# Kernel tuning notes

Hardware: AMD Instinct MI355X
Metric: run time of the kernel (lower is better)

The kernel has to match this reference:

```python
import jax, jax.numpy as jnp
import numpy as np

INF = 1e5
EPS = 1e-8
SCALE = 0.1            # coordinate_scaling
VFN_F = 1.0            # vfn_attn_factor
DIST_F = 1.0           # dist_attn_factor
AFS = VFN_F + DIST_F + 2.0  # attn_factor_sum
B, N, CS, H, C, P, PV, K, G = 2, 512, 384, 12, 16, 8, 8, 16, 64


def quat_to_rot(q):
    q = q / jnp.linalg.norm(q, axis=-1, keepdims=True)
    w, x, y, z = q[..., 0], q[..., 1], q[..., 2], q[..., 3]
    R = jnp.stack([
        1 - 2 * (y * y + z * z), 2 * (x * y - w * z), 2 * (x * z + w * y),
        2 * (x * y + w * z), 1 - 2 * (x * x + z * z), 2 * (y * z - w * x),
        2 * (x * z - w * y), 2 * (y * z + w * x), 1 - 2 * (x * x + y * y)], axis=-1)
    return R.reshape(q.shape[:-1] + (3, 3))


def layer_norm(x, g, b):
    m = jnp.mean(x, -1, keepdims=True)
    v = jnp.mean((x - m) ** 2, -1, keepdims=True)
    return (x - m) * jax.lax.rsqrt(v + 1e-5) * g + b


def setup_inputs() -> dict:
    key = jax.random.key(0)
    ks = jax.random.split(key, 32)
    w = lambda k, shape, sc=0.02: jax.random.normal(k, shape, jnp.float32) * sc
    s = jax.random.normal(ks[0], (B, N, CS), jnp.float32)
    rot = quat_to_rot(jax.random.normal(ks[1], (B, N, 4), jnp.float32))
    trans = jax.random.normal(ks[2], (B, N, 3), jnp.float32) * 10.0
    mask = jnp.ones((B, N), jnp.float32)
    return dict(
        s=s, rot=rot, trans=trans, mask=mask,
        Wq=w(ks[3], (CS, H * C)), bq=jnp.zeros((H * C,), jnp.float32),
        Wkv=w(ks[4], (CS, 2 * H * C)), bkv=jnp.zeros((2 * H * C,), jnp.float32),
        head_weights=jnp.full((H,), 0.5413, jnp.float32),
        ln_g=jnp.ones((CS,), jnp.float32), ln_b=jnp.zeros((CS,), jnp.float32),
        Wpq=w(ks[5], (CS, P * 3)), bpq=jnp.zeros((P * 3,), jnp.float32),
        Wpv=w(ks[6], (CS, P * 3)), bpv=jnp.zeros((P * 3,), jnp.float32),
        Wvl=w(ks[7], (P, 2 * P), 0.1),
        gbf_means=jnp.linspace(0.0, 3.0, K).astype(jnp.float32),
        gbf_stds=jnp.linspace(0.5, 2.0, K).astype(jnp.float32),
        Wg=w(ks[8], (P * K, G)), bg=jnp.zeros((G,), jnp.float32),
        W1=w(ks[9], (G, G)), b1=jnp.zeros((G,), jnp.float32),
        W2=w(ks[10], (G, H)), b2=jnp.zeros((H,), jnp.float32),
        Wkvp=w(ks[11], (CS, H * PV * 3)), bkvp=jnp.zeros((H * PV * 3,), jnp.float32),
        Wout=w(ks[12], (H * (C + 4 * PV), CS)), bout=jnp.zeros((CS,), jnp.float32),
    )


def reference(s, rot, trans, mask, Wq, bq, Wkv, bkv, head_weights, ln_g, ln_b,
              Wpq, bpq, Wpv, bpv, Wvl, gbf_means, gbf_stds, Wg, bg,
              W1, b1, W2, b2, Wkvp, bkvp, Wout, bout):
    # pairwise squared distances on scaled coordinates -> per-head distance bias
    coord = trans * SCALE
    diff = coord[:, None, :, :] - coord[:, :, None, :]
    pair_dist = jnp.sum(diff * diff, -1)                      # [B,N,N]
    hw = jax.nn.softplus(head_weights) * ((1.0 / (AFS * 4.5)) ** 0.5) * -0.5
    dist_att = pair_dist[..., None] * hw                      # [B,N,N,H]

    # scalar q/k/v
    q = (s @ Wq + bq).reshape(B, N, H, C)
    kv = (s @ Wkv + bkv).reshape(B, N, H, 2 * C)
    k, v = kv[..., :C], kv[..., C:]

    # VFN point features from layer-normed s
    sn = layer_norm(s, ln_g, ln_b)
    q_pts = (sn @ Wpq + bpq).reshape(B, N, P, 3)
    v_pts = (sn @ Wpv + bpv).reshape(B, N, P, 3)

    # relative rigid T_i^{-1} o T_j applied to v_pts of residue j
    R_rel = jnp.einsum('biyx,bjyz->bijxz', rot, rot)          # R_i^T R_j [B,N,N,3,3]
    dt = trans[:, None, :, :] - trans[:, :, None, :]          # t_j - t_i
    t_rel = jnp.einsum('biyx,bijy->bijx', rot, dt)            # R_i^T (t_j - t_i)
    v_loc = jnp.einsum('bijxy,bjpy->bijpx', R_rel, v_pts) + t_rel[:, :, :, None, :]
    q_rep = jnp.broadcast_to(q_pts[:, :, None], (B, N, N, P, 3))
    vin = jnp.concatenate([v_loc, q_rep], axis=-2)            # [B,N,N,2P,3]
    vec = jnp.einsum('op,bijpc->bijoc', Wvl, vin) + v_loc     # equivariant VecLinear + residual
    vlen = jnp.sqrt(jnp.sum(vec * vec, -1) + EPS)             # [B,N,N,P]

    # Gaussian basis expansion then pair MLP -> per-head VFN attention bias
    gauss = jnp.exp(-0.5 * ((vlen[..., None] - gbf_means) / gbf_stds) ** 2)  # [B,N,N,P,K]
    g = gauss.reshape(B, N, N, P * K) @ Wg + bg               # [B,N,N,G]
    vfn = jax.nn.relu(g @ W1 + b1) @ W2 + b2                  # [B,N,N,H]

    # fused attention logits
    a = jnp.einsum('bihc,bjhc->bhij', q, k) * ((1.0 / (AFS * C)) ** 0.5)
    a = a + jnp.transpose(vfn, (0, 3, 1, 2)) * (VFN_F / (AFS ** 0.5))
    a = a + jnp.transpose(dist_att, (0, 3, 1, 2)) * DIST_F
    sq_mask = INF * (mask[:, :, None] * mask[:, None, :] - 1.0)
    a = jax.nn.softmax(a + sq_mask[:, None], axis=-1)         # [B,H,N,N]

    # scalar output
    o = jnp.einsum('bhij,bjhc->bihc', a, v).reshape(B, N, H * C)

    # point values in global (scaled) frame, aggregate, back to local frame
    kv_pts = (s @ Wkvp + bkvp).reshape(B, N, H * PV, 3)
    ts = trans * SCALE
    vg = (jnp.einsum('bixy,biky->bikx', rot, kv_pts) + ts[:, :, None, :]).reshape(B, N, H, PV, 3)
    o_pt = jnp.einsum('bhij,bjhpc->bihpc', a, vg)             # [B,N,H,PV,3]
    o_loc = jnp.einsum('biyx,bihpy->bihpx', rot, o_pt - ts[:, :, None, None, :])
    dists = jnp.sqrt(jnp.sum(o_loc * o_loc, -1) + EPS).reshape(B, N, H * PV)
    pts = o_loc.reshape(B, N, H * PV, 3)
    feats = jnp.concatenate([o, pts[..., 0], pts[..., 1], pts[..., 2], dists], axis=-1)
    s_out = feats @ Wout + bout                               # [B,N,CS]
    return s_out, g
```

## Files before the change

### kernel.cpp

```cpp
#include <hip/hip_runtime.h>
#include <math.h>

#define BB 2
#define NN 512
#define CSZ 384
#define HH 12
#define CC 16
#define PP 8
#define PVV 8
#define KG 16
#define GG 64
#define NCOL 912
#define NODES (BB*NN)

typedef __attribute__((ext_vector_type(8))) short bf16x8;
typedef __attribute__((ext_vector_type(4))) float floatx4;

__device__ __forceinline__ unsigned short f2bf(float x) {
  unsigned u = __float_as_uint(x);
  unsigned r = (u + 0x7FFF + ((u >> 16) & 1)) >> 16;
  return (unsigned short)r;
}

__global__ void k0_prep(const float* __restrict__ Wq, const float* __restrict__ Wkv,
                        const float* __restrict__ Wpq, const float* __restrict__ Wpv,
                        const float* __restrict__ Wkvp,
                        const float* __restrict__ bq, const float* __restrict__ bkv,
                        const float* __restrict__ bpq, const float* __restrict__ bpv,
                        const float* __restrict__ bkvp,
                        const float* __restrict__ ln_g, const float* __restrict__ ln_b,
                        const float* __restrict__ W1, const float* __restrict__ hwin,
                        const float* __restrict__ Wg, const float* __restrict__ W2,
                        float* __restrict__ Wbig, float* __restrict__ biasbig,
                        float* __restrict__ P2big, unsigned short* __restrict__ wbf,
                        float* __restrict__ hw)
{
  int idx = blockIdx.x*blockDim.x + threadIdx.x;
  int stride = gridDim.x*blockDim.x;
  for (int t = idx; t < CSZ*NCOL; t += stride) {
    int f = t / NCOL, c = t % NCOL;
    float w;
    if (c < 192)      w = Wq[f*192 + c];
    else if (c < 576) w = Wkv[f*384 + (c-192)];
    else if (c < 600) w = ln_g[f]*Wpq[f*24 + (c-576)];
    else if (c < 624) w = ln_g[f]*Wpv[f*24 + (c-600)];
    else              w = Wkvp[f*288 + (c-624)];
    Wbig[t] = w;
  }
  for (int t = idx; t < 8192; t += stride) {
    int ch = t >> 7, pk = t & 127;
    float wv = Wg[pk*64 + ch];
    unsigned short h = f2bf(wv);
    float hf = __uint_as_float(((unsigned)h) << 16);
    wbf[t] = h;
    wbf[8192 + t] = f2bf(wv - hf);
  }
  for (int t = idx; t < 4096; t += stride) {
    int ho = t >> 6, k = t & 63;
    wbf[16384 + t] = f2bf(W1[k*64 + ho]);
  }
  for (int t = idx; t < 1024; t += stride) {
    int hh = t >> 6, ho = t & 63;
    wbf[20480 + t] = (hh < 12) ? f2bf(W2[ho*12 + hh]) : (unsigned short)0;
  }
  for (int c = idx; c < NCOL; c += stride) {
    float bb, p2 = 0.f;
    if (c < 192)      bb = bq[c];
    else if (c < 576) bb = bkv[c-192];
    else if (c < 624) {
      const float* W = (c < 600) ? (Wpq + (c-576)) : (Wpv + (c-600));
      float p1 = 0.f;
      for (int f = 0; f < CSZ; ++f) { p1 += ln_b[f]*W[f*24]; p2 += ln_g[f]*W[f*24]; }
      bb = ((c < 600) ? bpq[c-576] : bpv[c-600]) + p1;
    }
    else bb = bkvp[c-624];
    biasbig[c] = bb; P2big[c] = p2;
  }
  for (int h = idx; h < HH; h += stride) {
    float x = hwin[h];
    float sp = (x > 20.f) ? x : log1pf(expf(x));
    hw[h] = sp * sqrtf(1.0f/18.0f) * -0.5f;
  }
}

__global__ void k0b_stats(const float* __restrict__ s, float* __restrict__ mout,
                          float* __restrict__ rstdout)
{
  int node = blockIdx.x;
  int l = threadIdx.x;
  const float* row = s + node*CSZ;
  float sum = 0.f, sum2 = 0.f;
  for (int f = l; f < CSZ; f += 64) { float v = row[f]; sum += v; sum2 += v*v; }
  #pragma unroll
  for (int off = 1; off < 64; off <<= 1) { sum += __shfl_xor(sum, off); sum2 += __shfl_xor(sum2, off); }
  if (l == 0) {
    float m = sum / CSZ;
    float var = sum2 / CSZ - m*m;
    mout[node] = m;
    rstdout[node] = rsqrtf(var + 1e-5f);
  }
}

__launch_bounds__(256)
__global__ void k1_gemm(const float* __restrict__ s, const float* __restrict__ Wbig,
                        const float* __restrict__ biasbig, const float* __restrict__ P2big,
                        const float* __restrict__ mrow, const float* __restrict__ rstd,
                        float* __restrict__ act)
{
  const int ROWS = 4;
  int row0 = blockIdx.x * ROWS;
  int t = threadIdx.x;
  float acc[4][ROWS];
  #pragma unroll
  for (int j = 0; j < 4; ++j)
    #pragma unroll
    for (int r = 0; r < ROWS; ++r) acc[j][r] = 0.f;

  int c3 = t + 768;
  #pragma unroll 4
  for (int f = 0; f < CSZ; ++f) {
    const float* wrow = Wbig + f*NCOL;
    float w0 = wrow[t], w1 = wrow[t+256], w2 = wrow[t+512];
    float w3 = (c3 < NCOL) ? wrow[c3] : 0.f;
    #pragma unroll
    for (int r = 0; r < ROWS; ++r) {
      float sv = s[(row0+r)*CSZ + f];
      acc[0][r] = fmaf(sv, w0, acc[0][r]);
      acc[1][r] = fmaf(sv, w1, acc[1][r]);
      acc[2][r] = fmaf(sv, w2, acc[2][r]);
      acc[3][r] = fmaf(sv, w3, acc[3][r]);
    }
  }
  #pragma unroll
  for (int j = 0; j < 4; ++j) {
    int c = t + j*256;
    if (c < NCOL) {
      float bb = biasbig[c], p2v = P2big[c];
      bool lncol = (c >= 576 && c < 624);
      #pragma unroll
      for (int r = 0; r < ROWS; ++r) {
        int node = row0 + r;
        float v;
        if (lncol) { float rs = rstd[node]; v = acc[j][r]*rs + bb - mrow[node]*rs*p2v; }
        else       v = acc[j][r] + bb;
        act[node*NCOL + c] = v;
      }
    }
  }
}

__global__ void k1b_post(const float* __restrict__ act, const float* __restrict__ rot,
                         const float* __restrict__ trans,
                         float* __restrict__ vT, float* __restrict__ vgT)
{
  int idx = blockIdx.x*blockDim.x + threadIdx.x;
  const int NT1 = BB*HH*CC*NN;
  const int NT2 = BB*HH*PVV*3*NN;
  if (idx < NT1) {
    int n = idx & (NN-1); int rest = idx >> 9;
    int c = rest & 15; rest >>= 4;
    int h = rest % HH; int b = rest / HH;
    int node = b*NN + n;
    vT[idx] = act[node*NCOL + 192 + h*32 + 16 + c];
  } else if (idx < NT1 + NT2) {
    int j = idx - NT1;
    int n = j & (NN-1); int rest = j >> 9;
    int p3 = rest % 24; rest /= 24;
    int h = rest % HH; int b = rest / HH;
    int node = b*NN + n;
    int p = p3 / 3, x = p3 % 3;
    int hp = h*PVV + p;
    const float* kp = act + node*NCOL + 624 + hp*3;
    const float* R = rot + node*9;
    vgT[j] = R[x*3+0]*kp[0] + R[x*3+1]*kp[1] + R[x*3+2]*kp[2] + trans[node*3+x]*0.1f;
  }
}

__launch_bounds__(256, 2)
__global__ void k2_pair(const float* __restrict__ act, const float* __restrict__ rot,
                        const float* __restrict__ trans, const float* __restrict__ mask,
                        const float* __restrict__ Wvl, const float* __restrict__ gm_in,
                        const float* __restrict__ gs_in,
                        const unsigned short* __restrict__ wbf,
                        const float* __restrict__ bg, const float* __restrict__ b1,
                        const float* __restrict__ b2, const float* __restrict__ hw,
                        float* __restrict__ gout, float* __restrict__ apre)
{
  __shared__ __align__(16) unsigned short s_gauss[128*128];
  __shared__ __align__(16) unsigned short s_g[128*64];
  __shared__ float s_qvec[24];
  __shared__ float s_q[192];
  __shared__ float s_wvl[128];
  __shared__ float s_gm[KG], s_gis[KG];
  __shared__ float s_hw[HH];

  int bi = blockIdx.x;
  int b = bi >> 9, i = bi & (NN-1);
  int t = threadIdx.x;
  int w = t >> 6, l = t & 63;
  int lo = l & 15, hi4 = l >> 4;
  const float* acti = act + (size_t)bi*NCOL;

  if (t < 24) {
    int o = t / 3, c = t % 3;
    float sum = 0.f;
    #pragma unroll
    for (int p = 0; p < PP; ++p) sum += Wvl[o*16 + 8 + p] * acti[576 + p*3 + c];
    s_qvec[t] = sum;
  } else if (t >= 32 && t < 48) {
    int k = t - 32; s_gm[k] = gm_in[k]; s_gis[k] = 1.f / gs_in[k];
  } else if (t >= 64 && t < 76) {
    s_hw[t-64] = hw[t-64];
  }
  if (t < 192) s_q[t] = acti[t];
  if (t < 128) s_wvl[t] = Wvl[t];

  int n0 = w*16;
  bf16x8 wgf[8];
  #pragma unroll
  for (int kr = 0; kr < 4; ++kr) {
    int el = (n0+lo)*128 + kr*32 + hi4*8;
    wgf[kr*2+0] = *(const bf16x8*)(wbf + el);
    wgf[kr*2+1] = *(const bf16x8*)(wbf + 8192 + el);
  }
  bf16x8 w1f[2], w2f[2];
  #pragma unroll
  for (int kr = 0; kr < 2; ++kr) {
    w1f[kr] = *(const bf16x8*)(wbf + 16384 + (n0+lo)*64 + kr*32 + hi4*8);
    w2f[kr] = *(const bf16x8*)(wbf + 20480 + lo*64 + kr*32 + hi4*8);
  }

  float bgv = bg[n0 + lo];
  float b1v = b1[n0 + lo];
  int head = lo;
  float b2v = (head < 12) ? b2[head] : 0.f;
  float mi = mask[bi];
  float ti0 = trans[bi*3], ti1 = trans[bi*3+1], ti2 = trans[bi*3+2];
  float ri[9];
  #pragma unroll
  for (int q = 0; q < 9; ++q) ri[q] = rot[(size_t)bi*9 + q];
  __syncthreads();

  float hwv = s_hw[(head < 12) ? head : 0];
  float qv[16];
  {
    int hq = (head < 12) ? head : 0;
    #pragma unroll
    for (int c = 0; c < 16; ++c) qv[c] = s_q[hq*16 + c];
  }

  char* gb = (char*)s_gauss;
  char* sg = (char*)s_g;

  for (int tt = 0; tt < 4; ++tt) {
    int jt0 = tt*128;

    {
      int jo = t >> 1, kh = t & 1;
      int jnode = b*NN + jt0 + jo;
      const float* actj = act + (size_t)jnode*NCOL;
      float rj[9];
      #pragma unroll
      for (int q = 0; q < 9; ++q) rj[q] = rot[(size_t)jnode*9 + q];
      float d0 = trans[jnode*3]-ti0, d1 = trans[jnode*3+1]-ti1, d2 = trans[jnode*3+2]-ti2;
      float Rr[9];
      #pragma unroll
      for (int x = 0; x < 3; ++x)
        #pragma unroll
        for (int z = 0; z < 3; ++z)
          Rr[x*3+z] = ri[x]*rj[z] + ri[3+x]*rj[3+z] + ri[6+x]*rj[6+z];
      float tr[3];
      #pragma unroll
      for (int x = 0; x < 3; ++x) tr[x] = ri[x]*d0 + ri[3+x]*d1 + ri[6+x]*d2;
      float vpl[24];
      {
        const float4* v4 = (const float4*)(actj + 600);
        #pragma unroll
        for (int q = 0; q < 6; ++q) {
          float4 x4 = v4[q];
          vpl[q*4+0] = x4.x; vpl[q*4+1] = x4.y; vpl[q*4+2] = x4.z; vpl[q*4+3] = x4.w;
        }
      }
      #pragma unroll
      for (int p = 0; p < PP; ++p) {
        float x0 = vpl[p*3], x1 = vpl[p*3+1], x2 = vpl[p*3+2];
        float l0 = fmaf(Rr[0], x0, fmaf(Rr[1], x1, fmaf(Rr[2], x2, tr[0])));
        float l1 = fmaf(Rr[3], x0, fmaf(Rr[4], x1, fmaf(Rr[5], x2, tr[1])));
        float l2 = fmaf(Rr[6], x0, fmaf(Rr[7], x1, fmaf(Rr[8], x2, tr[2])));
        vpl[p*3] = l0; vpl[p*3+1] = l1; vpl[p*3+2] = l2;
      }
      #pragma unroll
      for (int oo = 0; oo < 4; ++oo) {
        int o = kh*4 + oo;
        float vx = vpl[o*3+0] + s_qvec[o*3+0];
        float vy = vpl[o*3+1] + s_qvec[o*3+1];
        float vz = vpl[o*3+2] + s_qvec[o*3+2];
        #pragma unroll
        for (int p = 0; p < PP; ++p) {
          float wv = s_wvl[o*16+p];
          vx = fmaf(wv, vpl[p*3+0], vx);
          vy = fmaf(wv, vpl[p*3+1], vy);
          vz = fmaf(wv, vpl[p*3+2], vz);
        }
        float vlen = sqrtf(vx*vx + vy*vy + vz*vz + 1e-8f);
        #pragma unroll
        for (int seg = 0; seg < 2; ++seg) {
          bf16x8 pk;
          #pragma unroll
          for (int e = 0; e < 8; ++e) {
            int kk = seg*8 + e;
            float tg = (vlen - s_gm[kk]) * s_gis[kk];
            pk[e] = (short)f2bf(__expf(-0.5f * tg * tg));
          }
          int byt = jo*256 + kh*128 + oo*32 + seg*16;
          byt ^= (jo & 7) << 4;
          *(bf16x8*)(gb + byt) = pk;
        }
      }
    }
    __syncthreads();

    #pragma unroll 1
    for (int m = 0; m < 8; ++m) {
      floatx4 ag = {bgv, bgv, bgv, bgv};
      #pragma unroll
      for (int kr = 0; kr < 4; ++kr) {
        int row = m*16 + lo;
        int byt = (row*256 + (kr*32 + hi4*8)*2) ^ ((row & 7) << 4);
        bf16x8 a = *(const bf16x8*)(gb + byt);
        ag = __builtin_amdgcn_mfma_f32_16x16x32_bf16(a, wgf[kr*2+0], ag, 0, 0, 0);
        ag = __builtin_amdgcn_mfma_f32_16x16x32_bf16(a, wgf[kr*2+1], ag, 0, 0, 0);
      }
      int jb = jt0 + m*16 + hi4*4;
      float* gp = gout + ((size_t)bi*NN + jb)*64 + (n0 + lo);
      #pragma unroll
      for (int r = 0; r < 4; ++r) gp[r*64] = ag[r];
      #pragma unroll
      for (int r = 0; r < 4; ++r) {
        int row = m*16 + hi4*4 + r;
        int byt = (row*128 + (n0 + lo)*2) ^ ((row & 7) << 4);
        *(unsigned short*)(sg + byt) = f2bf(ag[r]);
      }
    }
    __syncthreads();

    #pragma unroll 1
    for (int m = 0; m < 8; ++m) {
      floatx4 a0 = {b1v, b1v, b1v, b1v};
      #pragma unroll
      for (int kr = 0; kr < 2; ++kr) {
        int row = m*16 + lo;
        int byt = (row*128 + (kr*32 + hi4*8)*2) ^ ((row & 7) << 4);
        bf16x8 a = *(const bf16x8*)(sg + byt);
        a0 = __builtin_amdgcn_mfma_f32_16x16x32_bf16(a, w1f[kr], a0, 0, 0, 0);
      }
      #pragma unroll
      for (int r = 0; r < 4; ++r) {
        float v = fmaxf(a0[r], 0.f);
        int row = m*16 + hi4*4 + r;
        int byt = (row*128 + (n0 + lo)*2) ^ ((row & 7) << 4);
        *(unsigned short*)(gb + byt) = f2bf(v);
      }
    }
    __syncthreads();

    #pragma unroll 1
    for (int mm = 0; mm < 2; ++mm) {
      int m = w*2 + mm;
      floatx4 av = {b2v, b2v, b2v, b2v};
      #pragma unroll
      for (int kr = 0; kr < 2; ++kr) {
        int row = m*16 + lo;
        int byt = (row*128 + (kr*32 + hi4*8)*2) ^ ((row & 7) << 4);
        bf16x8 a = *(const bf16x8*)(gb + byt);
        av = __builtin_amdgcn_mfma_f32_16x16x32_bf16(a, w2f[kr], av, 0, 0, 0);
      }
      if (head < 12) {
        int jb = jt0 + m*16 + hi4*4;
        #pragma unroll
        for (int r = 0; r < 4; ++r) {
          int j = jb + r, jnode = b*NN + j;
          const float4* k4 = (const float4*)(act + (size_t)jnode*NCOL + 192 + head*16);
          float4 ka = k4[0], kb = k4[1], kc = k4[2], kd = k4[3];
          float qk = qv[0]*ka.x;
          qk = fmaf(qv[1], ka.y, qk);  qk = fmaf(qv[2], ka.z, qk);  qk = fmaf(qv[3], ka.w, qk);
          qk = fmaf(qv[4], kb.x, qk);  qk = fmaf(qv[5], kb.y, qk);  qk = fmaf(qv[6], kb.z, qk);
          qk = fmaf(qv[7], kb.w, qk);  qk = fmaf(qv[8], kc.x, qk);  qk = fmaf(qv[9], kc.y, qk);
          qk = fmaf(qv[10], kc.z, qk); qk = fmaf(qv[11], kc.w, qk); qk = fmaf(qv[12], kd.x, qk);
          qk = fmaf(qv[13], kd.y, qk); qk = fmaf(qv[14], kd.z, qk); qk = fmaf(qv[15], kd.w, qk);
          float d0 = trans[jnode*3]-ti0, d1 = trans[jnode*3+1]-ti1, d2 = trans[jnode*3+2]-ti2;
          float pd = 0.01f*(d0*d0 + d1*d1 + d2*d2);
          float mt = 100000.f*(mi*mask[jnode] - 1.f);
          apre[(((size_t)b*HH + head)*NN + i)*NN + j] = qk*0.125f + av[r]*0.5f + pd*hwv + mt;
        }
      }
    }
    __syncthreads();
  }
}

__launch_bounds__(256)
__global__ void k3_attend(const float* __restrict__ apre, const float* __restrict__ vT,
                          const float* __restrict__ vgT,
                          float* __restrict__ oout, float* __restrict__ optout)
{
  __shared__ float a4t[4][NN];
  int blk = blockIdx.x;
  int ic = blk & 127; int rest = blk >> 7;
  int h = rest % HH; int b = rest / HH;
  int i0 = ic * 4;
  int t = threadIdx.x; int w = t >> 6; int l = t & 63;

  {
    int i = i0 + w;
    const float* row = apre + (((size_t)b*HH + h)*NN + i)*NN;
    float vals[8];
    float m = -1e30f;
    #pragma unroll
    for (int s8 = 0; s8 < 8; ++s8) { vals[s8] = row[l + 64*s8]; m = fmaxf(m, vals[s8]); }
    #pragma unroll
    for (int off = 1; off < 64; off <<= 1) m = fmaxf(m, __shfl_xor(m, off));
    float sum = 0.f;
    #pragma unroll
    for (int s8 = 0; s8 < 8; ++s8) { vals[s8] = __expf(vals[s8] - m); sum += vals[s8]; }
    #pragma unroll
    for (int off = 1; off < 64; off <<= 1) sum += __shfl_xor(sum, off);
    float inv = 1.f / sum;
    #pragma unroll
    for (int s8 = 0; s8 < 8; ++s8) a4t[w][l + 64*s8] = vals[s8] * inv;
  }
  __syncthreads();

  const float* vbase = vT + ((size_t)(b*HH + h)*CC)*NN;
  const float* gbase = vgT + ((size_t)(b*HH + h)*24)*NN;
  #pragma unroll 1
  for (int pass = 0; pass < 5; ++pass) {
    int c0 = w + 8*pass;
    int c1 = c0 + 4;
    const float* s0 = (c0 < 16) ? (vbase + c0*NN) : (gbase + (c0-16)*NN);
    const float* s1 = (c1 < 16) ? (vbase + c1*NN) : (gbase + (c1-16)*NN);
    float acc0[4] = {0,0,0,0}, acc1[4] = {0,0,0,0};
    #pragma unroll
    for (int s8 = 0; s8 < 8; ++s8) {
      int j = l + 64*s8;
      float a0 = a4t[0][j], a1 = a4t[1][j], a2 = a4t[2][j], a3 = a4t[3][j];
      float v0 = s0[j], v1 = s1[j];
      acc0[0] = fmaf(a0, v0, acc0[0]); acc0[1] = fmaf(a1, v0, acc0[1]);
      acc0[2] = fmaf(a2, v0, acc0[2]); acc0[3] = fmaf(a3, v0, acc0[3]);
      acc1[0] = fmaf(a0, v1, acc1[0]); acc1[1] = fmaf(a1, v1, acc1[1]);
      acc1[2] = fmaf(a2, v1, acc1[2]); acc1[3] = fmaf(a3, v1, acc1[3]);
    }
    #pragma unroll
    for (int r = 0; r < 4; ++r) {
      #pragma unroll
      for (int off = 1; off < 64; off <<= 1) {
        acc0[r] += __shfl_xor(acc0[r], off);
        acc1[r] += __shfl_xor(acc1[r], off);
      }
    }
    if (l == 0) {
      #pragma unroll
      for (int r = 0; r < 4; ++r) {
        int node = b*NN + i0 + r;
        if (c0 < 16) oout[node*192 + h*16 + c0] = acc0[r];
        else         optout[node*288 + h*24 + (c0-16)] = acc0[r];
        if (c1 < 16) oout[node*192 + h*16 + c1] = acc1[r];
        else         optout[node*288 + h*24 + (c1-16)] = acc1[r];
      }
    }
  }
}

__global__ void k4a_feats(const float* __restrict__ oo, const float* __restrict__ opt,
                          const float* __restrict__ rot, const float* __restrict__ trans,
                          float* __restrict__ feats)
{
  int node = blockIdx.x; int t = threadIdx.x;
  float* fr = feats + node*576;
  if (t < 192) {
    fr[t] = oo[node*192 + t];
  } else if (t < 288) {
    int hp = t - 192;
    const float* R = rot + node*9;
    float tx = trans[node*3+0]*0.1f, ty = trans[node*3+1]*0.1f, tz = trans[node*3+2]*0.1f;
    const float* op = opt + (node*96 + hp)*3;
    float px = op[0]-tx, py = op[1]-ty, pz = op[2]-tz;
    float lx = R[0]*px + R[3]*py + R[6]*pz;
    float ly = R[1]*px + R[4]*py + R[7]*pz;
    float lz = R[2]*px + R[5]*py + R[8]*pz;
    float d = sqrtf(lx*lx + ly*ly + lz*lz + 1e-8f);
    fr[192+hp] = lx; fr[288+hp] = ly; fr[384+hp] = lz; fr[480+hp] = d;
  }
}

__launch_bounds__(384)
__global__ void k4b_out(const float* __restrict__ feats, const float* __restrict__ Wout,
                        const float* __restrict__ bout, float* __restrict__ sout)
{
  const int ROWS = 4;
  int row0 = blockIdx.x * ROWS;
  int c = threadIdx.x;
  float acc[ROWS];
  #pragma unroll
  for (int r = 0; r < ROWS; ++r) acc[r] = 0.f;
  #pragma unroll 4
  for (int f = 0; f < 576; ++f) {
    float wv = Wout[f*384 + c];
    #pragma unroll
    for (int r = 0; r < ROWS; ++r)
      acc[r] = fmaf(feats[(row0+r)*576 + f], wv, acc[r]);
  }
  float bb = bout[c];
  #pragma unroll
  for (int r = 0; r < ROWS; ++r) sout[(row0+r)*384 + c] = acc[r] + bb;
}

extern "C" void kernel_launch(void* const* d_in, const int* in_sizes, int n_in,
                              void* d_out, int out_size, void* d_ws, size_t ws_size,
                              hipStream_t stream)
{
  const float* s     = (const float*)d_in[0];
  const float* rot   = (const float*)d_in[1];
  const float* trans = (const float*)d_in[2];
  const float* mask  = (const float*)d_in[3];
  const float* Wq    = (const float*)d_in[4];
  const float* bq    = (const float*)d_in[5];
  const float* Wkv   = (const float*)d_in[6];
  const float* bkv   = (const float*)d_in[7];
  const float* hwts  = (const float*)d_in[8];
  const float* ln_g  = (const float*)d_in[9];
  const float* ln_b  = (const float*)d_in[10];
  const float* Wpq   = (const float*)d_in[11];
  const float* bpq   = (const float*)d_in[12];
  const float* Wpv   = (const float*)d_in[13];
  const float* bpv   = (const float*)d_in[14];
  const float* Wvl   = (const float*)d_in[15];
  const float* gbm   = (const float*)d_in[16];
  const float* gbs   = (const float*)d_in[17];
  const float* Wg    = (const float*)d_in[18];
  const float* bg    = (const float*)d_in[19];
  const float* W1    = (const float*)d_in[20];
  const float* b1    = (const float*)d_in[21];
  const float* W2    = (const float*)d_in[22];
  const float* b2    = (const float*)d_in[23];
  const float* Wkvp  = (const float*)d_in[24];
  const float* bkvp  = (const float*)d_in[25];
  const float* Wout  = (const float*)d_in[26];
  const float* bout  = (const float*)d_in[27];

  float* ws = (float*)d_ws;
  float* act   = ws + 0;
  float* Wbig  = ws + 933888;
  float* bias  = ws + 1284096;
  float* P2    = ws + 1285008;
  float* W1T   = ws + 1285920;
  float* hw    = ws + 1290016;
  float* mrow  = ws + 1290032;
  float* rstd  = ws + 1291056;
  float* vT    = ws + 1292080;
  float* vgT   = ws + 1488688;
  float* apre  = ws + 1783600;
  float* oo    = ws + 8075056;
  float* opt   = ws + 8271664;
  float* feats = ws + 8566576;
  unsigned short* wbf = (unsigned short*)(ws + 9156400);

  float* sout = (float*)d_out;
  float* gout = sout + BB*NN*CSZ;

  (void)W1T;

  hipLaunchKernelGGL(k0_prep, dim3(256), dim3(256), 0, stream,
                     Wq, Wkv, Wpq, Wpv, Wkvp, bq, bkv, bpq, bpv, bkvp,
                     ln_g, ln_b, W1, hwts, Wg, W2, Wbig, bias, P2, wbf, hw);
  hipLaunchKernelGGL(k0b_stats, dim3(1024), dim3(64), 0, stream, s, mrow, rstd);
  hipLaunchKernelGGL(k1_gemm, dim3(256), dim3(256), 0, stream,
                     s, Wbig, bias, P2, mrow, rstd, act);
  hipLaunchKernelGGL(k1b_post, dim3(1920), dim3(256), 0, stream, act, rot, trans, vT, vgT);
  hipLaunchKernelGGL(k2_pair, dim3(1024), dim3(256), 0, stream,
                     act, rot, trans, mask, Wvl, gbm, gbs, wbf, bg, b1, b2, hw,
                     gout, apre);
  hipLaunchKernelGGL(k3_attend, dim3(3072), dim3(256), 0, stream, apre, vT, vgT, oo, opt);
  hipLaunchKernelGGL(k4a_feats, dim3(1024), dim3(320), 0, stream, oo, opt, rot, trans, feats);
  hipLaunchKernelGGL(k4b_out, dim3(256), dim3(384), 0, stream, feats, Wout, bout, sout);
}
```

Measured before the change: 454.0 us.

## Use bf16 MFMA for attention-value aggregation and parallelize LN bias folding

The attention aggregation kernel now handles 16 query rows per block. It stores the softmax probabilities as bf16 in swizzled shared memory and computes the weighted sum over values and point values with 16x16x32 bf16 MFMA, replacing scalar FMAs and shuffle reductions. The value and global-point tensors are repacked into one bf16 buffer padded to 48 channels, which halves their memory traffic. The prep kernel folds the layer-norm weights into the bias with one wave per column instead of a serial loop, and the output GEMM gets hoisted row pointers. The trade-off is bf16 rounding of both the attention weights and the values, which lowers accuracy.

```diff
diff --git a/kernel.cpp b/kernel.cpp
--- a/kernel.cpp
+++ b/kernel.cpp
@@ -63,18 +63,32 @@
     int hh = t >> 6, ho = t & 63;
     wbf[20480 + t] = (hh < 12) ? f2bf(W2[ho*12 + hh]) : (unsigned short)0;
   }
+  {
+    int wid = idx >> 6, lane = idx & 63;
+    if (wid < 48) {
+      int c = 576 + wid;
+      const float* W = (c < 600) ? (Wpq + (c-576)) : (Wpv + (c-600));
+      float p1 = 0.f, p2 = 0.f;
+      for (int f = lane; f < CSZ; f += 64) {
+        float wv = W[f*24];
+        p1 = fmaf(ln_b[f], wv, p1);
+        p2 = fmaf(ln_g[f], wv, p2);
+      }
+      #pragma unroll
+      for (int off = 1; off < 64; off <<= 1) { p1 += __shfl_xor(p1, off); p2 += __shfl_xor(p2, off); }
+      if (lane == 0) {
+        biasbig[c] = ((c < 600) ? bpq[c-576] : bpv[c-600]) + p1;
+        P2big[c] = p2;
+      }
+    }
+  }
   for (int c = idx; c < NCOL; c += stride) {
-    float bb, p2 = 0.f;
+    if (c >= 576 && c < 624) continue;
+    float bb;
     if (c < 192)      bb = bq[c];
     else if (c < 576) bb = bkv[c-192];
-    else if (c < 624) {
-      const float* W = (c < 600) ? (Wpq + (c-576)) : (Wpv + (c-600));
-      float p1 = 0.f;
-      for (int f = 0; f < CSZ; ++f) { p1 += ln_b[f]*W[f*24]; p2 += ln_g[f]*W[f*24]; }
-      bb = ((c < 600) ? bpq[c-576] : bpv[c-600]) + p1;
-    }
-    else bb = bkvp[c-624];
-    biasbig[c] = bb; P2big[c] = p2;
+    else              bb = bkvp[c-624];
+    biasbig[c] = bb; P2big[c] = 0.f;
   }
   for (int h = idx; h < HH; h += stride) {
     float x = hwin[h];
@@ -151,29 +165,29 @@
 
 __global__ void k1b_post(const float* __restrict__ act, const float* __restrict__ rot,
                          const float* __restrict__ trans,
-                         float* __restrict__ vT, float* __restrict__ vgT)
+                         unsigned short* __restrict__ vbf)
 {
   int idx = blockIdx.x*blockDim.x + threadIdx.x;
-  const int NT1 = BB*HH*CC*NN;
-  const int NT2 = BB*HH*PVV*3*NN;
-  if (idx < NT1) {
-    int n = idx & (NN-1); int rest = idx >> 9;
-    int c = rest & 15; rest >>= 4;
-    int h = rest % HH; int b = rest / HH;
-    int node = b*NN + n;
-    vT[idx] = act[node*NCOL + 192 + h*32 + 16 + c];
-  } else if (idx < NT1 + NT2) {
-    int j = idx - NT1;
-    int n = j & (NN-1); int rest = j >> 9;
-    int p3 = rest % 24; rest /= 24;
-    int h = rest % HH; int b = rest / HH;
-    int node = b*NN + n;
+  const int NT = 24*48*512;
+  if (idx >= NT) return;
+  int j = idx & 511; int rest = idx >> 9;
+  int c = rest % 48; int bh = rest / 48;
+  int h = bh % HH, b = bh / HH;
+  int node = b*NN + j;
+  float v;
+  if (c < 16) {
+    v = act[(size_t)node*NCOL + 192 + h*32 + 16 + c];
+  } else if (c < 40) {
+    int p3 = c - 16;
     int p = p3 / 3, x = p3 % 3;
     int hp = h*PVV + p;
-    const float* kp = act + node*NCOL + 624 + hp*3;
+    const float* kp = act + (size_t)node*NCOL + 624 + hp*3;
     const float* R = rot + node*9;
-    vgT[j] = R[x*3+0]*kp[0] + R[x*3+1]*kp[1] + R[x*3+2]*kp[2] + trans[node*3+x]*0.1f;
-  }
+    v = R[x*3+0]*kp[0] + R[x*3+1]*kp[1] + R[x*3+2]*kp[2] + trans[node*3+x]*0.1f;
+  } else {
+    v = 0.f;
+  }
+  vbf[idx] = f2bf(v);
 }
 
 __launch_bounds__(256, 2)
@@ -400,20 +414,24 @@
 }
 
 __launch_bounds__(256)
-__global__ void k3_attend(const float* __restrict__ apre, const float* __restrict__ vT,
-                          const float* __restrict__ vgT,
+__global__ void k3_attend(const float* __restrict__ apre, const unsigned short* __restrict__ vbf,
                           float* __restrict__ oout, float* __restrict__ optout)
 {
-  __shared__ float a4t[4][NN];
+  __shared__ __align__(16) unsigned short s_a[16*512];
+  __shared__ __align__(16) float s_red[12*256];
   int blk = blockIdx.x;
-  int ic = blk & 127; int rest = blk >> 7;
-  int h = rest % HH; int b = rest / HH;
-  int i0 = ic * 4;
+  int itile = blk & 31; int bh = blk >> 5;
+  int h = bh % HH, b = bh / HH;
+  int i0 = itile*16;
   int t = threadIdx.x; int w = t >> 6; int l = t & 63;
-
-  {
-    int i = i0 + w;
-    const float* row = apre + (((size_t)b*HH + h)*NN + i)*NN;
+  int lo = l & 15, hi4 = l >> 4;
+
+  const float* rowbase = apre + ((size_t)bh*NN + i0)*NN;
+
+  #pragma unroll 1
+  for (int rr = 0; rr < 4; ++rr) {
+    int il = rr*4 + w;
+    const float* row = rowbase + (size_t)il*NN;
     float vals[8];
     float m = -1e30f;
     #pragma unroll
@@ -427,46 +445,46 @@
     for (int off = 1; off < 64; off <<= 1) sum += __shfl_xor(sum, off);
     float inv = 1.f / sum;
     #pragma unroll
-    for (int s8 = 0; s8 < 8; ++s8) a4t[w][l + 64*s8] = vals[s8] * inv;
-  }
-  __syncthreads();
-
-  const float* vbase = vT + ((size_t)(b*HH + h)*CC)*NN;
-  const float* gbase = vgT + ((size_t)(b*HH + h)*24)*NN;
-  #pragma unroll 1
-  for (int pass = 0; pass < 5; ++pass) {
-    int c0 = w + 8*pass;
-    int c1 = c0 + 4;
-    const float* s0 = (c0 < 16) ? (vbase + c0*NN) : (gbase + (c0-16)*NN);
-    const float* s1 = (c1 < 16) ? (vbase + c1*NN) : (gbase + (c1-16)*NN);
-    float acc0[4] = {0,0,0,0}, acc1[4] = {0,0,0,0};
-    #pragma unroll
     for (int s8 = 0; s8 < 8; ++s8) {
       int j = l + 64*s8;
-      float a0 = a4t[0][j], a1 = a4t[1][j], a2 = a4t[2][j], a3 = a4t[3][j];
-      float v0 = s0[j], v1 = s1[j];
-      acc0[0] = fmaf(a0, v0, acc0[0]); acc0[1] = fmaf(a1, v0, acc0[1]);
-      acc0[2] = fmaf(a2, v0, acc0[2]); acc0[3] = fmaf(a3, v0, acc0[3]);
-      acc1[0] = fmaf(a0, v1, acc1[0]); acc1[1] = fmaf(a1, v1, acc1[1]);
-      acc1[2] = fmaf(a2, v1, acc1[2]); acc1[3] = fmaf(a3, v1, acc1[3]);
-    }
+      int byt = (il*1024 + j*2) ^ ((il & 7) << 4);
+      *(unsigned short*)((char*)s_a + byt) = f2bf(vals[s8] * inv);
+    }
+  }
+  __syncthreads();
+
+  const unsigned short* vb = vbf + (size_t)bh*48*512;
+  floatx4 acc[3];
+  #pragma unroll
+  for (int n = 0; n < 3; ++n) acc[n] = (floatx4){0.f, 0.f, 0.f, 0.f};
+  #pragma unroll 1
+  for (int ks = 0; ks < 4; ++ks) {
+    int k0 = w*128 + ks*32;
+    int abyte = (lo*1024 + (k0 + hi4*8)*2) ^ ((lo & 7) << 4);
+    bf16x8 af = *(const bf16x8*)((char*)s_a + abyte);
+    #pragma unroll
+    for (int n = 0; n < 3; ++n) {
+      bf16x8 bf = *(const bf16x8*)(vb + (n*16 + lo)*512 + k0 + hi4*8);
+      acc[n] = __builtin_amdgcn_mfma_f32_16x16x32_bf16(af, bf, acc[n], 0, 0, 0);
+    }
+  }
+  #pragma unroll
+  for (int n = 0; n < 3; ++n)
+    *(floatx4*)&s_red[((w*3 + n) << 8) + (l << 2)] = acc[n];
+  __syncthreads();
+
+  if (w < 3) {
+    floatx4 o0 = *(const floatx4*)&s_red[((0*3 + w) << 8) + (l << 2)];
+    floatx4 o1 = *(const floatx4*)&s_red[((1*3 + w) << 8) + (l << 2)];
+    floatx4 o2 = *(const floatx4*)&s_red[((2*3 + w) << 8) + (l << 2)];
+    floatx4 o3 = *(const floatx4*)&s_red[((3*3 + w) << 8) + (l << 2)];
+    int c = w*16 + lo;
     #pragma unroll
     for (int r = 0; r < 4; ++r) {
-      #pragma unroll
-      for (int off = 1; off < 64; off <<= 1) {
-        acc0[r] += __shfl_xor(acc0[r], off);
-        acc1[r] += __shfl_xor(acc1[r], off);
-      }
-    }
-    if (l == 0) {
-      #pragma unroll
-      for (int r = 0; r < 4; ++r) {
-        int node = b*NN + i0 + r;
-        if (c0 < 16) oout[node*192 + h*16 + c0] = acc0[r];
-        else         optout[node*288 + h*24 + (c0-16)] = acc0[r];
-        if (c1 < 16) oout[node*192 + h*16 + c1] = acc1[r];
-        else         optout[node*288 + h*24 + (c1-16)] = acc1[r];
-      }
+      float val = (o0[r] + o1[r]) + (o2[r] + o3[r]);
+      int node = b*NN + i0 + hi4*4 + r;
+      if (c < 16)      oout[node*192 + h*16 + c] = val;
+      else if (c < 40) optout[node*288 + h*24 + (c-16)] = val;
     }
   }
 }
@@ -500,15 +518,21 @@
   const int ROWS = 4;
   int row0 = blockIdx.x * ROWS;
   int c = threadIdx.x;
+  int zz; asm volatile("v_mov_b32 %0, 0" : "=v"(zz));
+  const float* f0 = feats + (row0+0)*576 + zz;
+  const float* f1 = feats + (row0+1)*576 + zz;
+  const float* f2 = feats + (row0+2)*576 + zz;
+  const float* f3 = feats + (row0+3)*576 + zz;
   float acc[ROWS];
   #pragma unroll
   for (int r = 0; r < ROWS; ++r) acc[r] = 0.f;
   #pragma unroll 4
   for (int f = 0; f < 576; ++f) {
     float wv = Wout[f*384 + c];
-    #pragma unroll
-    for (int r = 0; r < ROWS; ++r)
-      acc[r] = fmaf(feats[(row0+r)*576 + f], wv, acc[r]);
+    acc[0] = fmaf(f0[f], wv, acc[0]);
+    acc[1] = fmaf(f1[f], wv, acc[1]);
+    acc[2] = fmaf(f2[f], wv, acc[2]);
+    acc[3] = fmaf(f3[f], wv, acc[3]);
   }
   float bb = bout[c];
   #pragma unroll
@@ -553,12 +577,10 @@
   float* Wbig  = ws + 933888;
   float* bias  = ws + 1284096;
   float* P2    = ws + 1285008;
-  float* W1T   = ws + 1285920;
   float* hw    = ws + 1290016;
   float* mrow  = ws + 1290032;
   float* rstd  = ws + 1291056;
-  float* vT    = ws + 1292080;
-  float* vgT   = ws + 1488688;
+  unsigned short* vbf = (unsigned short*)(ws + 1292080);
   float* apre  = ws + 1783600;
   float* oo    = ws + 8075056;
   float* opt   = ws + 8271664;
@@ -567,8 +589,6 @@
 
   float* sout = (float*)d_out;
   float* gout = sout + BB*NN*CSZ;
-
-  (void)W1T;
 
   hipLaunchKernelGGL(k0_prep, dim3(256), dim3(256), 0, stream,
                      Wq, Wkv, Wpq, Wpv, Wkvp, bq, bkv, bpq, bpv, bkvp,
@@ -576,11 +596,11 @@
   hipLaunchKernelGGL(k0b_stats, dim3(1024), dim3(64), 0, stream, s, mrow, rstd);
   hipLaunchKernelGGL(k1_gemm, dim3(256), dim3(256), 0, stream,
                      s, Wbig, bias, P2, mrow, rstd, act);
-  hipLaunchKernelGGL(k1b_post, dim3(1920), dim3(256), 0, stream, act, rot, trans, vT, vgT);
+  hipLaunchKernelGGL(k1b_post, dim3(2304), dim3(256), 0, stream, act, rot, trans, vbf);
   hipLaunchKernelGGL(k2_pair, dim3(1024), dim3(256), 0, stream,
                      act, rot, trans, mask, Wvl, gbm, gbs, wbf, bg, b1, b2, hw,
                      gout, apre);
-  hipLaunchKernelGGL(k3_attend, dim3(3072), dim3(256), 0, stream, apre, vT, vgT, oo, opt);
+  hipLaunchKernelGGL(k3_attend, dim3(768), dim3(256), 0, stream, apre, vbf, oo, opt);
   hipLaunchKernelGGL(k4a_feats, dim3(1024), dim3(320), 0, stream, oo, opt, rot, trans, feats);
   hipLaunchKernelGGL(k4b_out, dim3(256), dim3(384), 0, stream, feats, Wout, bout, sout);
 }
```

New measurement: 420.3 us. 7.4% less time.
